# Optimization experiments

Measured on AMD Instinct MI355X. Metric: run time of the kernel, lower is better.

## Reference

```python
import jax, jax.numpy as jnp
import numpy as np


def _squash(s, axis=-1, eps=1e-8):
    # squash(s) = |s|^2/(1+|s|^2) * s/|s|
    s2 = jnp.sum(s * s, axis=axis, keepdims=True)
    return (s2 / (1.0 + s2)) * s / jnp.sqrt(s2 + eps)


def _conv(x, w, b, stride):
    y = jax.lax.conv_general_dilated(
        x, w, (stride, stride), 'VALID',
        dimension_numbers=('NCHW', 'OIHW', 'NCHW'))
    return y + b[None, :, None, None]


def setup_inputs() -> dict:
    key = jax.random.key(0)
    ks = jax.random.split(key, 4)
    B = 64
    sc = 0.05
    return {
        'x': jax.random.normal(ks[0], (B, 3, 32, 32), jnp.float32),
        'conv_w': jax.random.normal(ks[1], (256, 3, 9, 9), jnp.float32) * sc,
        'conv_b': jnp.zeros((256,), jnp.float32),
        'pcap_w': jax.random.normal(ks[2], (256, 256, 9, 9), jnp.float32) * sc,
        'pcap_b': jnp.zeros((256,), jnp.float32),
        'W': jax.random.normal(ks[3], (100, 2048, 16, 8), jnp.float32) * sc,
    }


def reference(x, conv_w, conv_b, pcap_w, pcap_b, W):
    # Conv stem: [B,3,32,32] -> [B,256,24,24]
    h = jax.nn.relu(_conv(x, conv_w, conv_b, 1))
    # PrimaryCaps conv: [B,256,24,24] -> [B,256,8,8], then view to capsules
    p = _conv(h, pcap_w, pcap_b, 2)
    u = _squash(p.reshape(p.shape[0], 2048, 8))            # [B,2048,8]
    # DenseCapsule: u_hat[b,o,i,d] = W[o,i,d,k] u[b,i,k]
    u_hat = jnp.einsum('oidk,bik->boid', W, u)             # [B,100,2048,16]
    u_hat_sg = jax.lax.stop_gradient(u_hat)
    b = jnp.zeros(u_hat.shape[:3], u_hat.dtype)            # [B,100,2048]
    routings = 3
    v = None
    for i in range(routings):
        c = jax.nn.softmax(b, axis=1)                      # over out caps
        uh = u_hat if i == routings - 1 else u_hat_sg
        v = _squash(jnp.einsum('boi,boid->bod', c, uh))    # [B,100,16]
        if i < routings - 1:
            b = b + jnp.einsum('bod,boid->boi', v, u_hat_sg)
    return v
```

## Files before the change

### kernel.cpp

```cpp
#include <hip/hip_runtime.h>

#define NB 64
#define NO 100
#define NI 2048
#define ND 16
#define NK 8

#define WS_H    0
#define WS_U    9437184
#define WS_BB   10485760
#define WS_CB   23592960
#define WS_SP   36700160
#define WS_V    38338560
#define WS_PP   WS_BB

typedef __attribute__((ext_vector_type(8))) short bf16x8;
typedef __attribute__((ext_vector_type(16))) float f32x16;
typedef __attribute__((ext_vector_type(4))) float f32x4;

__device__ inline unsigned short f2bf(float x) {
    union { float f; unsigned u; } v; v.f = x;
    unsigned r = (v.u + 0x7FFFu + ((v.u >> 16) & 1u)) >> 16;
    return (unsigned short)r;
}
__device__ inline float bf2f(unsigned short h) {
    union { unsigned u; float f; } v; v.u = ((unsigned)h) << 16;
    return v.f;
}

__global__ __launch_bounds__(256) void conv1_kernel(const float* __restrict__ x,
        const float* __restrict__ w, const float* __restrict__ bias,
        unsigned short* __restrict__ h_hi, unsigned short* __restrict__ h_lo) {
    const int b = blockIdx.x;
    const int ocg = blockIdx.y;
    __shared__ float xl[3 * 32 * 32];
    __shared__ float wl[16 * 243];
    const int tid = threadIdx.x;
    for (int idx = tid; idx < 3072; idx += 256) xl[idx] = x[b * 3072 + idx];
    for (int idx = tid; idx < 16 * 243; idx += 256)
        wl[idx] = w[ocg * 16 * 243 + idx];
    __syncthreads();
    const int lane = tid & 63;
    const int wg = tid >> 6;
    float acc[4][9];
    #pragma unroll
    for (int jj = 0; jj < 4; ++jj) {
        float bv = bias[ocg * 16 + wg * 4 + jj];
        #pragma unroll
        for (int j = 0; j < 9; ++j) acc[jj][j] = bv;
    }
    int xbase[9];
    #pragma unroll
    for (int j = 0; j < 9; ++j) {
        int p = lane + 64 * j;
        xbase[j] = (p / 24) * 32 + (p % 24);
    }
    for (int ic = 0; ic < 3; ++ic)
        for (int ky = 0; ky < 9; ++ky) {
            #pragma unroll
            for (int kx = 0; kx < 9; ++kx) {
                float wv[4];
                #pragma unroll
                for (int jj = 0; jj < 4; ++jj)
                    wv[jj] = wl[(wg * 4 + jj) * 243 + ic * 81 + ky * 9 + kx];
                #pragma unroll
                for (int j = 0; j < 9; ++j) {
                    float xv = xl[ic * 1024 + xbase[j] + ky * 32 + kx];
                    #pragma unroll
                    for (int jj = 0; jj < 4; ++jj)
                        acc[jj][j] = fmaf(xv, wv[jj], acc[jj][j]);
                }
            }
        }
    #pragma unroll
    for (int jj = 0; jj < 4; ++jj) {
        int oc = ocg * 16 + wg * 4 + jj;
        #pragma unroll
        for (int j = 0; j < 9; ++j) {
            int p = lane + 64 * j;
            float v = fmaxf(acc[jj][j], 0.f);
            unsigned short hi = f2bf(v);
            unsigned short lo = f2bf(v - bf2f(hi));
            size_t o = (size_t)(b * 256 + oc) * 576 + p;
            h_hi[o] = hi;
            h_lo[o] = lo;
        }
    }
}

__global__ __launch_bounds__(256) void wb_precompute_kernel(const float* __restrict__ w,
        unsigned short* __restrict__ wBhi, unsigned short* __restrict__ wBlo) {
    const int ic = blockIdx.x;
    const int ocq = blockIdx.y;
    __shared__ float tl[64][85];
    const int tid = threadIdx.x;
    for (int f = tid; f < 5184; f += 256) {
        int oc = f / 81, kk = f % 81;
        tl[oc][kk] = w[(size_t)(ocq * 64 + oc) * 20736 + ic * 81 + kk];
    }
    __syncthreads();
    for (int idx = tid; idx < 9216; idx += 256) {
        int ky = idx >> 10;
        int rem = idx & 1023;
        int ocl = rem >> 4;
        int kx = rem & 15;
        float val = (kx < 9) ? tl[ocl][ky * 9 + kx] : 0.f;
        unsigned short hi = f2bf(val);
        unsigned short lo = f2bf(val - bf2f(hi));
        size_t dst = ((size_t)(ic * 9 + ky) * 256 + ocq * 64 + ocl) * 16 + kx;
        wBhi[dst] = hi;
        wBlo[dst] = lo;
    }
}

__global__ __launch_bounds__(256) void conv2_mfma_kernel(
        const unsigned short* __restrict__ h_hi, const unsigned short* __restrict__ h_lo,
        const unsigned short* __restrict__ wBhi, const unsigned short* __restrict__ wBlo,
        float* __restrict__ pp) {
    const int bpair = blockIdx.x;
    const int ocb = blockIdx.y;
    const int ks = blockIdx.z;
    __shared__ __align__(16) unsigned short Ahi[128 * 16];
    __shared__ __align__(16) unsigned short Alo[128 * 16];
    __shared__ __align__(16) unsigned short Bhi[128 * 16];
    __shared__ __align__(16) unsigned short Blo[128 * 16];
    const int tid = threadIdx.x;
    const int lane = tid & 63;
    const int wid = tid >> 6;
    const int wr = wid >> 1, wc = wid & 1;
    const int l31 = lane & 31, kh = lane >> 5;
    const int slot = tid & 127;
    const int role = tid >> 7;
    const int oy = (slot >> 3) & 7;
    const int ox = slot & 7;
    const unsigned short* hsel = role ? h_lo : h_hi;
    const size_t hrow0 = ((size_t)(bpair * 2 + (slot >> 6)) * 256) * 576;

    f32x16 acc[2][2];
    #pragma unroll
    for (int m = 0; m < 2; ++m)
        #pragma unroll
        for (int n = 0; n < 2; ++n)
            #pragma unroll
            for (int r = 0; r < 16; ++r) acc[m][n][r] = 0.f;

    const int ic0 = ks * 32;
    for (int ic = ic0; ic < ic0 + 32; ++ic) {
        const size_t wb_ic = (size_t)ic * 9 * 4096;
        const size_t h_ic = hrow0 + (size_t)ic * 576;
        #pragma unroll 1
        for (int ky = 0; ky < 9; ++ky) {
            __syncthreads();
            const uint4* Ash = (const uint4*)(wBhi + wb_ic + (size_t)ky * 4096 + ocb * 2048);
            const uint4* Asl = (const uint4*)(wBlo + wb_ic + (size_t)ky * 4096 + ocb * 2048);
            ((uint4*)Ahi)[tid] = Ash[tid];
            ((uint4*)Alo)[tid] = Asl[tid];
            const unsigned int* hp =
                (const unsigned int*)(hsel + h_ic + (2 * oy + ky) * 24 + 2 * ox);
            unsigned int d0 = hp[0], d1 = hp[1], d2 = hp[2], d3 = hp[3], d4 = hp[4];
            unsigned short* Bdst = (role ? Blo : Bhi) + slot * 16;
            uint4 w0; w0.x = d0; w0.y = d1; w0.z = d2; w0.w = d3;
            uint4 w1; w1.x = d4 & 0xFFFFu; w1.y = 0u; w1.z = 0u; w1.w = 0u;
            *(uint4*)Bdst = w0;
            *(uint4*)(Bdst + 8) = w1;
            __syncthreads();
            bf16x8 ah[2], al[2], bh[2], bl[2];
            #pragma unroll
            for (int m = 0; m < 2; ++m) {
                const int rowoff = (wr * 64 + m * 32 + l31) * 16 + kh * 8;
                ah[m] = *(const bf16x8*)&Ahi[rowoff];
                al[m] = *(const bf16x8*)&Alo[rowoff];
            }
            #pragma unroll
            for (int n = 0; n < 2; ++n) {
                const int coloff = (wc * 64 + n * 32 + l31) * 16 + kh * 8;
                bh[n] = *(const bf16x8*)&Bhi[coloff];
                bl[n] = *(const bf16x8*)&Blo[coloff];
            }
            #pragma unroll
            for (int m = 0; m < 2; ++m)
                #pragma unroll
                for (int n = 0; n < 2; ++n) {
                    acc[m][n] = __builtin_amdgcn_mfma_f32_32x32x16_bf16(
                        ah[m], bh[n], acc[m][n], 0, 0, 0);
                    acc[m][n] = __builtin_amdgcn_mfma_f32_32x32x16_bf16(
                        ah[m], bl[n], acc[m][n], 0, 0, 0);
                    acc[m][n] = __builtin_amdgcn_mfma_f32_32x32x16_bf16(
                        al[m], bh[n], acc[m][n], 0, 0, 0);
                }
        }
    }
    #pragma unroll
    for (int m = 0; m < 2; ++m)
        #pragma unroll
        for (int n = 0; n < 2; ++n) {
            const int slotg = wc * 64 + n * 32 + l31;
            const int b = bpair * 2 + (slotg >> 6);
            const int pos = slotg & 63;
            #pragma unroll
            for (int r = 0; r < 16; ++r) {
                const int row = (r & 3) + 8 * (r >> 2) + 4 * kh;
                const int oc = ocb * 128 + wr * 64 + m * 32 + row;
                pp[(((size_t)ks * 64 + b) * 256 + oc) * 64 + pos] = acc[m][n][r];
            }
        }
}

__global__ __launch_bounds__(256) void reduce_bias_squash_kernel(
        const float* __restrict__ pp, const float* __restrict__ bias,
        float* __restrict__ u) {
    const int cap = blockIdx.x * 256 + threadIdx.x;
    const int b = cap >> 11;
    const int rem = cap & 2047;
    const int oc = rem >> 3;
    const int oy = rem & 7;
    float4 sa = {0.f, 0.f, 0.f, 0.f}, sb = {0.f, 0.f, 0.f, 0.f};
    #pragma unroll
    for (int ks = 0; ks < 8; ++ks) {
        const float4* p4 = (const float4*)&pp[(((size_t)ks * 64 + b) * 256 + oc) * 64 + oy * 8];
        float4 a = p4[0], c = p4[1];
        sa.x += a.x; sa.y += a.y; sa.z += a.z; sa.w += a.w;
        sb.x += c.x; sb.y += c.y; sb.z += c.z; sb.w += c.w;
    }
    const float bv = bias[oc];
    sa.x += bv; sa.y += bv; sa.z += bv; sa.w += bv;
    sb.x += bv; sb.y += bv; sb.z += bv; sb.w += bv;
    float s2 = sa.x * sa.x + sa.y * sa.y + sa.z * sa.z + sa.w * sa.w
             + sb.x * sb.x + sb.y * sb.y + sb.z * sb.z + sb.w * sb.w;
    float scale = (s2 / (1.f + s2)) / sqrtf(s2 + 1e-8f);
    sa.x *= scale; sa.y *= scale; sa.z *= scale; sa.w *= scale;
    sb.x *= scale; sb.y *= scale; sb.z *= scale; sb.w *= scale;
    float4* up = (float4*)&u[(size_t)cap * 8];
    up[0] = sa;
    up[1] = sb;
}

__global__ __launch_bounds__(256) void transpose_u_kernel(const float* __restrict__ u,
        float* __restrict__ ut) {
    const int blk = blockIdx.x;
    __shared__ float tl[64 * 132];
    const int tid = threadIdx.x;
    #pragma unroll
    for (int rep = 0; rep < 8; ++rep) {
        const int idx = tid + 256 * rep;
        const int b = idx >> 5, q = idx & 31;
        float4 uv = *(const float4*)(u + (size_t)b * 16384 + blk * 128 + 4 * q);
        *(float4*)&tl[b * 132 + 4 * q] = uv;
    }
    __syncthreads();
    #pragma unroll
    for (int rep = 0; rep < 32; ++rep) {
        const int row = rep * 4 + (tid >> 6);
        const int b = tid & 63;
        ut[(size_t)(blk * 128 + row) * 64 + b] = tl[b * 132 + row];
    }
}

template <int UNIFORM>
__global__ __launch_bounds__(256) void r_weighted_mfma_kernel(
        const float* __restrict__ W, const float* __restrict__ u,
        const float* __restrict__ cbuf, float* __restrict__ sp) {
    const int o = blockIdx.x;
    const int st = blockIdx.y;
    __shared__ __align__(16) unsigned short Ahi[16 * 72];
    __shared__ __align__(16) unsigned short Alo[16 * 72];
    __shared__ __align__(16) unsigned short Bhi[64 * 72];
    __shared__ __align__(16) unsigned short Blo[64 * 72];
    const int tid = threadIdx.x;
    const int lane = tid & 63;
    const int w = tid >> 6;
    const int l15 = lane & 15;
    const int hi = lane >> 4;
    const int sb = tid >> 2;
    const int si = tid & 3;
    f32x4 acc = {0.f, 0.f, 0.f, 0.f};
    const float* Wo = W + (size_t)o * 262144;
    const int i_base = st * 256;
    #pragma unroll 1
    for (int iter = 0; iter < 32; ++iter) {
        const int i0 = i_base + iter * 8;
        __syncthreads();
        {
            float4 wv = *(const float4*)(Wo + (size_t)i0 * 128 + 4 * tid);
            const int i_l = tid >> 5;
            const int d = (tid >> 1) & 15;
            const int k0 = (tid & 1) * 4;
            unsigned short* dh = Ahi + d * 72 + i_l * 8 + k0;
            unsigned short* dl = Alo + d * 72 + i_l * 8 + k0;
            float vv[4] = {wv.x, wv.y, wv.z, wv.w};
            unsigned int h01, h23, l01, l23;
            unsigned short h, l;
            h = f2bf(vv[0]); l = f2bf(vv[0] - bf2f(h)); h01 = h; l01 = l;
            h = f2bf(vv[1]); l = f2bf(vv[1] - bf2f(h)); h01 |= (unsigned)h << 16; l01 |= (unsigned)l << 16;
            h = f2bf(vv[2]); l = f2bf(vv[2] - bf2f(h)); h23 = h; l23 = l;
            h = f2bf(vv[3]); l = f2bf(vv[3] - bf2f(h)); h23 |= (unsigned)h << 16; l23 |= (unsigned)l << 16;
            *(unsigned int*)dh = h01; *(unsigned int*)(dh + 2) = h23;
            *(unsigned int*)dl = l01; *(unsigned int*)(dl + 2) = l23;
        }
        #pragma unroll
        for (int half = 0; half < 2; ++half) {
            const int i_l = si + 4 * half;
            const float* up = u + (size_t)sb * 16384 + (size_t)(i0 + i_l) * 8;
            float4 u0 = *(const float4*)up;
            float4 u1 = *(const float4*)(up + 4);
            float cv = UNIFORM ? 0.01f
                               : cbuf[(size_t)sb * (NO * NI) + o * NI + i0 + i_l];
            float q[8] = {u0.x * cv, u0.y * cv, u0.z * cv, u0.w * cv,
                          u1.x * cv, u1.y * cv, u1.z * cv, u1.w * cv};
            uint4 ph, pl;
            unsigned short h0, h1, l0, l1;
            h0 = f2bf(q[0]); l0 = f2bf(q[0] - bf2f(h0));
            h1 = f2bf(q[1]); l1 = f2bf(q[1] - bf2f(h1));
            ph.x = h0 | ((unsigned)h1 << 16); pl.x = l0 | ((unsigned)l1 << 16);
            h0 = f2bf(q[2]); l0 = f2bf(q[2] - bf2f(h0));
            h1 = f2bf(q[3]); l1 = f2bf(q[3] - bf2f(h1));
            ph.y = h0 | ((unsigned)h1 << 16); pl.y = l0 | ((unsigned)l1 << 16);
            h0 = f2bf(q[4]); l0 = f2bf(q[4] - bf2f(h0));
            h1 = f2bf(q[5]); l1 = f2bf(q[5] - bf2f(h1));
            ph.z = h0 | ((unsigned)h1 << 16); pl.z = l0 | ((unsigned)l1 << 16);
            h0 = f2bf(q[6]); l0 = f2bf(q[6] - bf2f(h0));
            h1 = f2bf(q[7]); l1 = f2bf(q[7] - bf2f(h1));
            ph.w = h0 | ((unsigned)h1 << 16); pl.w = l0 | ((unsigned)l1 << 16);
            *(uint4*)(Bhi + sb * 72 + i_l * 8) = ph;
            *(uint4*)(Blo + sb * 72 + i_l * 8) = pl;
        }
        __syncthreads();
        #pragma unroll
        for (int ch = 0; ch < 2; ++ch) {
            bf16x8 ah = *(const bf16x8*)(Ahi + l15 * 72 + ch * 32 + hi * 8);
            bf16x8 al = *(const bf16x8*)(Alo + l15 * 72 + ch * 32 + hi * 8);
            bf16x8 bh = *(const bf16x8*)(Bhi + (w * 16 + l15) * 72 + ch * 32 + hi * 8);
            bf16x8 bl = *(const bf16x8*)(Blo + (w * 16 + l15) * 72 + ch * 32 + hi * 8);
            acc = __builtin_amdgcn_mfma_f32_16x16x32_bf16(ah, bh, acc, 0, 0, 0);
            acc = __builtin_amdgcn_mfma_f32_16x16x32_bf16(ah, bl, acc, 0, 0, 0);
            acc = __builtin_amdgcn_mfma_f32_16x16x32_bf16(al, bh, acc, 0, 0, 0);
        }
    }
    const int bg = w * 16 + l15;
    float4 st4;
    st4.x = acc[0]; st4.y = acc[1]; st4.z = acc[2]; st4.w = acc[3];
    *(float4*)&sp[(((size_t)o * 8 + st) * 64 + bg) * 16 + hi * 4] = st4;
}

__global__ __launch_bounds__(256) void squash_v_kernel(const float* __restrict__ sp,
        float* __restrict__ dest) {
    const int t = blockIdx.x * 256 + threadIdx.x;
    const int d = t & 15;
    const int cap = t >> 4;
    const int o = cap >> 6;
    const int bb = cap & 63;
    float s = 0.f;
    #pragma unroll
    for (int st = 0; st < 8; ++st)
        s += sp[(((size_t)o * 8 + st) * 64 + bb) * 16 + d];
    float s2 = s * s;
    #pragma unroll
    for (int off = 1; off < 16; off <<= 1)
        s2 += __shfl_xor(s2, off, 16);
    float scale = (s2 / (1.f + s2)) / sqrtf(s2 + 1e-8f);
    dest[(bb * NO + o) * ND + d] = s * scale;
}

template <int ADD>
__global__ __launch_bounds__(256) void r_logits_mfma_kernel(
        const float* __restrict__ W, const float* __restrict__ ut,
        const float* __restrict__ v, float* __restrict__ bbuf) {
    const int o = blockIdx.x;
    const int st = blockIdx.y;
    __shared__ __align__(16) unsigned short Aext[128 * 40];
    __shared__ __align__(16) unsigned short B1[64 * 40];
    __shared__ __align__(16) unsigned short B2[64 * 40];
    __shared__ float ul[128 * 66];
    const int tid = threadIdx.x;
    const int lane = tid & 63;
    const int w = tid >> 6;
    const int l15 = lane & 15;
    const int hi = lane >> 4;
    const float* Wo = W + (size_t)o * 262144;
    {
        const int b = tid >> 2;
        const int dq = (tid & 3) * 4;
        float4 vv = *(const float4*)&v[((size_t)b * NO + o) * ND + dq];
        float q[4] = {vv.x, vv.y, vv.z, vv.w};
        #pragma unroll
        for (int c = 0; c < 4; ++c) {
            unsigned short h = f2bf(q[c]);
            unsigned short l = f2bf(q[c] - bf2f(h));
            B1[b * 40 + dq + c] = h;
            B1[b * 40 + 16 + dq + c] = h;
            B2[b * 40 + dq + c] = l;
            B2[b * 40 + 16 + dq + c] = 0;
        }
    }
    __syncthreads();
    #pragma unroll 1
    for (int iter = 0; iter < 8; ++iter) {
        __syncthreads();
        #pragma unroll
        for (int rep = 0; rep < 2; ++rep) {
            const int off = 4 * tid + 1024 * rep;
            float4 wv = *(const float4*)(Wo + (size_t)(st * 128 + iter * 16) * 128 + off);
            const int i_l = off >> 7;
            const int d = (off >> 3) & 15;
            const int k0 = off & 7;
            float va[4] = {wv.x, wv.y, wv.z, wv.w};
            #pragma unroll
            for (int c = 0; c < 4; ++c) {
                unsigned short h = f2bf(va[c]);
                unsigned short l = f2bf(va[c] - bf2f(h));
                const int row = i_l * 8 + k0 + c;
                Aext[row * 40 + d] = h;
                Aext[row * 40 + 16 + d] = l;
            }
        }
        const int base_row = (st * 128 + iter * 16) * 8;
        #pragma unroll
        for (int rep = 0; rep < 8; ++rep) {
            const int idx = tid + 256 * rep;
            const int row = idx >> 4, bq = idx & 15;
            float4 uv = *(const float4*)(ut + (size_t)(base_row + row) * 64 + 4 * bq);
            *(float4*)&ul[row * 66 + 4 * bq] = uv;
        }
        __syncthreads();
        f32x4 acc[8];
        bf16x8 bf1 = *(const bf16x8*)&B1[(w * 16 + l15) * 40 + hi * 8];
        bf16x8 bf2 = *(const bf16x8*)&B2[(w * 16 + l15) * 40 + hi * 8];
        #pragma unroll
        for (int mt = 0; mt < 8; ++mt) {
            f32x4 z = {0.f, 0.f, 0.f, 0.f};
            bf16x8 af = *(const bf16x8*)&Aext[(mt * 16 + l15) * 40 + hi * 8];
            z = __builtin_amdgcn_mfma_f32_16x16x32_bf16(af, bf1, z, 0, 0, 0);
            z = __builtin_amdgcn_mfma_f32_16x16x32_bf16(af, bf2, z, 0, 0, 0);
            acc[mt] = z;
        }
        #pragma unroll
        for (int mt = 0; mt < 8; ++mt) {
            float partial = 0.f;
            #pragma unroll
            for (int r = 0; r < 4; ++r) {
                const int grow = mt * 16 + hi * 4 + r;
                partial = fmaf(acc[mt][r], ul[grow * 66 + w * 16 + l15], partial);
            }
            float sum = partial + __shfl_xor(partial, 16);
            if ((hi & 1) == 0) {
                const int i_glob = st * 128 + iter * 16 + mt * 2 + (hi >> 1);
                const int bg = w * 16 + l15;
                const size_t addr = (size_t)bg * (NO * NI) + (size_t)o * NI + i_glob;
                bbuf[addr] = (ADD ? bbuf[addr] : 0.f) + sum;
            }
        }
    }
}

__global__ __launch_bounds__(256) void softmax_kernel(const float* __restrict__ bbuf,
        float* __restrict__ cbuf) {
    const int bb = blockIdx.x >> 3;
    const int i = (blockIdx.x & 7) * 256 + threadIdx.x;
    const float* col = bbuf + bb * (NO * NI) + i;
    float m = -1e30f;
    for (int o = 0; o < NO; ++o) m = fmaxf(m, col[o * NI]);
    float s = 0.f;
    for (int o = 0; o < NO; ++o) s += __expf(col[o * NI] - m);
    const float inv = 1.f / s;
    float* outp = cbuf + bb * (NO * NI) + i;
    for (int o = 0; o < NO; ++o) outp[o * NI] = __expf(col[o * NI] - m) * inv;
}

extern "C" void kernel_launch(void* const* d_in, const int* in_sizes, int n_in,
                              void* d_out, int out_size, void* d_ws, size_t ws_size,
                              hipStream_t stream) {
    (void)in_sizes; (void)n_in; (void)out_size; (void)ws_size;
    const float* x      = (const float*)d_in[0];
    const float* conv_w = (const float*)d_in[1];
    const float* conv_b = (const float*)d_in[2];
    const float* pcap_w = (const float*)d_in[3];
    const float* pcap_b = (const float*)d_in[4];
    const float* W      = (const float*)d_in[5];
    float* out = (float*)d_out;
    float* ws  = (float*)d_ws;
    unsigned short* h_hi = (unsigned short*)(ws + WS_H);
    unsigned short* h_lo = h_hi + 9437184;
    unsigned short* wBhi = (unsigned short*)(ws + WS_CB);
    unsigned short* wBlo = wBhi + 9437184;
    float* ut  = ws + WS_H;
    float* u   = ws + WS_U;
    float* bbf = ws + WS_BB;
    float* cbf = ws + WS_CB;
    float* sp  = ws + WS_SP;
    float* v   = ws + WS_V;
    float* pp  = ws + WS_PP;

    wb_precompute_kernel<<<dim3(256, 4), 256, 0, stream>>>(pcap_w, wBhi, wBlo);
    conv1_kernel<<<dim3(64, 16), 256, 0, stream>>>(x, conv_w, conv_b, h_hi, h_lo);
    conv2_mfma_kernel<<<dim3(32, 2, 8), 256, 0, stream>>>(h_hi, h_lo, wBhi, wBlo, pp);
    reduce_bias_squash_kernel<<<512, 256, 0, stream>>>(pp, pcap_b, u);
    transpose_u_kernel<<<128, 256, 0, stream>>>(u, ut);
    r_weighted_mfma_kernel<1><<<dim3(100, 8), 256, 0, stream>>>(W, u, nullptr, sp);
    squash_v_kernel<<<400, 256, 0, stream>>>(sp, v);
    r_logits_mfma_kernel<0><<<dim3(100, 16), 256, 0, stream>>>(W, ut, v, bbf);
    softmax_kernel<<<512, 256, 0, stream>>>(bbf, cbf);
    r_weighted_mfma_kernel<0><<<dim3(100, 8), 256, 0, stream>>>(W, u, cbf, sp);
    squash_v_kernel<<<400, 256, 0, stream>>>(sp, v);
    r_logits_mfma_kernel<1><<<dim3(100, 16), 256, 0, stream>>>(W, ut, v, bbf);
    softmax_kernel<<<512, 256, 0, stream>>>(bbf, cbf);
    r_weighted_mfma_kernel<0><<<dim3(100, 8), 256, 0, stream>>>(W, u, cbf, sp);
    squash_v_kernel<<<400, 256, 0, stream>>>(sp, out);
}
```

Baseline: 832.6 us.

## Double-buffer conv2 B tiles in LDS and load A fragments directly from global

Restructures the primary-capsule conv MFMA loop into a flattened 288-step software pipeline with two LDS buffers for the input (B) tile, so global loads for the next step overlap the MFMAs of the current one. Weight (A) fragments are no longer staged through shared memory and are instead read straight from global memory into registers, one step ahead. This aims to hide global-load latency and cut LDS traffic and barrier stalls, at the cost of more registers and uncoalesced-per-wave global weight reads that depend on cache hits.

```diff
diff --git a/kernel.cpp b/kernel.cpp
--- a/kernel.cpp
+++ b/kernel.cpp
@@ -120,10 +120,8 @@
     const int bpair = blockIdx.x;
     const int ocb = blockIdx.y;
     const int ks = blockIdx.z;
-    __shared__ __align__(16) unsigned short Ahi[128 * 16];
-    __shared__ __align__(16) unsigned short Alo[128 * 16];
-    __shared__ __align__(16) unsigned short Bhi[128 * 16];
-    __shared__ __align__(16) unsigned short Blo[128 * 16];
+    __shared__ __align__(16) unsigned short Bh[2][128 * 16];
+    __shared__ __align__(16) unsigned short Bl[2][128 * 16];
     const int tid = threadIdx.x;
     const int lane = tid & 63;
     const int wid = tid >> 6;
@@ -135,6 +133,12 @@
     const int ox = slot & 7;
     const unsigned short* hsel = role ? h_lo : h_hi;
     const size_t hrow0 = ((size_t)(bpair * 2 + (slot >> 6)) * 256) * 576;
+    const int ic0 = ks * 32;
+
+    const int aoff0 = (wr * 64 + l31) * 16 + kh * 8;
+    const int aoff1 = aoff0 + 512;
+    const int boff0 = (wc * 64 + l31) * 16 + kh * 8;
+    const int boff1 = boff0 + 512;
 
     f32x16 acc[2][2];
     #pragma unroll
@@ -144,66 +148,81 @@
             #pragma unroll
             for (int r = 0; r < 16; ++r) acc[m][n][r] = 0.f;
 
-    const int ic0 = ks * 32;
-    for (int ic = ic0; ic < ic0 + 32; ++ic) {
-        const size_t wb_ic = (size_t)ic * 9 * 4096;
-        const size_t h_ic = hrow0 + (size_t)ic * 576;
-        #pragma unroll 1
-        for (int ky = 0; ky < 9; ++ky) {
-            __syncthreads();
-            const uint4* Ash = (const uint4*)(wBhi + wb_ic + (size_t)ky * 4096 + ocb * 2048);
-            const uint4* Asl = (const uint4*)(wBlo + wb_ic + (size_t)ky * 4096 + ocb * 2048);
-            ((uint4*)Ahi)[tid] = Ash[tid];
-            ((uint4*)Alo)[tid] = Asl[tid];
-            const unsigned int* hp =
-                (const unsigned int*)(hsel + h_ic + (2 * oy + ky) * 24 + 2 * ox);
-            unsigned int d0 = hp[0], d1 = hp[1], d2 = hp[2], d3 = hp[3], d4 = hp[4];
-            unsigned short* Bdst = (role ? Blo : Bhi) + slot * 16;
-            uint4 w0; w0.x = d0; w0.y = d1; w0.z = d2; w0.w = d3;
-            uint4 w1; w1.x = d4 & 0xFFFFu; w1.y = 0u; w1.z = 0u; w1.w = 0u;
-            *(uint4*)Bdst = w0;
-            *(uint4*)(Bdst + 8) = w1;
-            __syncthreads();
-            bf16x8 ah[2], al[2], bh[2], bl[2];
-            #pragma unroll
-            for (int m = 0; m < 2; ++m) {
-                const int rowoff = (wr * 64 + m * 32 + l31) * 16 + kh * 8;
-                ah[m] = *(const bf16x8*)&Ahi[rowoff];
-                al[m] = *(const bf16x8*)&Alo[rowoff];
-            }
-            #pragma unroll
-            for (int n = 0; n < 2; ++n) {
-                const int coloff = (wc * 64 + n * 32 + l31) * 16 + kh * 8;
-                bh[n] = *(const bf16x8*)&Bhi[coloff];
-                bl[n] = *(const bf16x8*)&Blo[coloff];
-            }
-            #pragma unroll
-            for (int m = 0; m < 2; ++m)
-                #pragma unroll
-                for (int n = 0; n < 2; ++n) {
-                    acc[m][n] = __builtin_amdgcn_mfma_f32_32x32x16_bf16(
-                        ah[m], bh[n], acc[m][n], 0, 0, 0);
-                    acc[m][n] = __builtin_amdgcn_mfma_f32_32x32x16_bf16(
-                        ah[m], bl[n], acc[m][n], 0, 0, 0);
-                    acc[m][n] = __builtin_amdgcn_mfma_f32_32x32x16_bf16(
-                        al[m], bh[n], acc[m][n], 0, 0, 0);
-                }
-        }
-    }
+    unsigned int d0, d1, d2, d3, d4;
+
+#define GLOADB(c) { const int ic_ = ic0 + (c) / 9, ky_ = (c) % 9;                          \
+    const unsigned int* hp_ = (const unsigned int*)(hsel + hrow0 + (size_t)ic_ * 576       \
+        + (2 * oy + ky_) * 24 + 2 * ox);                                                   \
+    d0 = hp_[0]; d1 = hp_[1]; d2 = hp_[2]; d3 = hp_[3]; d4 = hp_[4]; }
+#define STOREB(buf) { unsigned short* Bdst_ = (role ? Bl[buf] : Bh[buf]) + slot * 16;      \
+    uint4 w0_; w0_.x = d0; w0_.y = d1; w0_.z = d2; w0_.w = d3;                             \
+    uint4 w1_; w1_.x = d4 & 0xFFFFu; w1_.y = 0u; w1_.z = 0u; w1_.w = 0u;                   \
+    *(uint4*)Bdst_ = w0_; *(uint4*)(Bdst_ + 8) = w1_; }
+#define LOADA(c, AH, AL) { const int ic_ = ic0 + (c) / 9, ky_ = (c) % 9;                   \
+    const size_t base_ = (size_t)ic_ * 36864 + (size_t)ky_ * 4096 + ocb * 2048;            \
+    AH[0] = *(const bf16x8*)(wBhi + base_ + aoff0);                                        \
+    AH[1] = *(const bf16x8*)(wBhi + base_ + aoff1);                                        \
+    AL[0] = *(const bf16x8*)(wBlo + base_ + aoff0);                                        \
+    AL[1] = *(const bf16x8*)(wBlo + base_ + aoff1); }
+#define MFMA12(AH, AL, buf) {                                                              \
+    bf16x8 bh0 = *(const bf16x8*)&Bh[buf][boff0];                                          \
+    bf16x8 bh1 = *(const bf16x8*)&Bh[buf][boff1];                                          \
+    bf16x8 bl0 = *(const bf16x8*)&Bl[buf][boff0];                                          \
+    bf16x8 bl1 = *(const bf16x8*)&Bl[buf][boff1];                                          \
+    acc[0][0] = __builtin_amdgcn_mfma_f32_32x32x16_bf16(AH[0], bh0, acc[0][0], 0, 0, 0);   \
+    acc[0][0] = __builtin_amdgcn_mfma_f32_32x32x16_bf16(AH[0], bl0, acc[0][0], 0, 0, 0);   \
+    acc[0][0] = __builtin_amdgcn_mfma_f32_32x32x16_bf16(AL[0], bh0, acc[0][0], 0, 0, 0);   \
+    acc[0][1] = __builtin_amdgcn_mfma_f32_32x32x16_bf16(AH[0], bh1, acc[0][1], 0, 0, 0);   \
+    acc[0][1] = __builtin_amdgcn_mfma_f32_32x32x16_bf16(AH[0], bl1, acc[0][1], 0, 0, 0);   \
+    acc[0][1] = __builtin_amdgcn_mfma_f32_32x32x16_bf16(AL[0], bh1, acc[0][1], 0, 0, 0);   \
+    acc[1][0] = __builtin_amdgcn_mfma_f32_32x32x16_bf16(AH[1], bh0, acc[1][0], 0, 0, 0);   \
+    acc[1][0] = __builtin_amdgcn_mfma_f32_32x32x16_bf16(AH[1], bl0, acc[1][0], 0, 0, 0);   \
+    acc[1][0] = __builtin_amdgcn_mfma_f32_32x32x16_bf16(AL[1], bh0, acc[1][0], 0, 0, 0);   \
+    acc[1][1] = __builtin_amdgcn_mfma_f32_32x32x16_bf16(AH[1], bh1, acc[1][1], 0, 0, 0);   \
+    acc[1][1] = __builtin_amdgcn_mfma_f32_32x32x16_bf16(AH[1], bl1, acc[1][1], 0, 0, 0);   \
+    acc[1][1] = __builtin_amdgcn_mfma_f32_32x32x16_bf16(AL[1], bh1, acc[1][1], 0, 0, 0); }
+
+    bf16x8 a0h[2], a0l[2], a1h[2], a1l[2];
+    GLOADB(0); STOREB(0);
+    GLOADB(1);
+    LOADA(0, a0h, a0l);
+    __syncthreads();
+    #pragma unroll 1
+    for (int c = 0; c < 288; c += 2) {
+        LOADA(c + 1, a1h, a1l);
+        MFMA12(a0h, a0l, 0);
+        STOREB(1);
+        if (c + 2 < 288) GLOADB(c + 2);
+        __syncthreads();
+        if (c + 2 < 288) LOADA(c + 2, a0h, a0l);
+        MFMA12(a1h, a1l, 1);
+        if (c + 2 < 288) {
+            STOREB(0);
+            GLOADB(c + 3);
+        }
+        __syncthreads();
+    }
+#undef GLOADB
+#undef STOREB
+#undef LOADA
+#undef MFMA12
+
+    const int b = bpair * 2 + ((wc * 64 + l31) >> 6);
     #pragma unroll
     for (int m = 0; m < 2; ++m)
         #pragma unroll
         for (int n = 0; n < 2; ++n) {
             const int slotg = wc * 64 + n * 32 + l31;
-            const int b = bpair * 2 + (slotg >> 6);
+            const int bb = bpair * 2 + (slotg >> 6);
             const int pos = slotg & 63;
             #pragma unroll
             for (int r = 0; r < 16; ++r) {
                 const int row = (r & 3) + 8 * (r >> 2) + 4 * kh;
                 const int oc = ocb * 128 + wr * 64 + m * 32 + row;
-                pp[(((size_t)ks * 64 + b) * 256 + oc) * 64 + pos] = acc[m][n][r];
+                pp[(((size_t)ks * 64 + bb) * 256 + oc) * 64 + pos] = acc[m][n][r];
             }
         }
+    (void)b;
 }
 
 __global__ __launch_bounds__(256) void reduce_bias_squash_kernel(
```

Result: slower. 850.8 us (+2.2%).
